# Kernel tuning notes

Hardware: AMD Instinct MI355X
Metric: run time of the kernel (lower is better)

## Reference

```python
import jax, jax.numpy as jnp
import numpy as np

NUM_QUBITS = 24
NUM_QUBITS_GATE = 2
NUM_STEPS = 8
GATE_DIM = 2 ** NUM_QUBITS_GATE  # 4


def setup_inputs() -> dict:
    key = jax.random.key(0)
    k1, k2 = jax.random.split(key)
    # state: stacked (real, imag) parts, shape (2,) + (2,)*NUM_QUBITS
    state = jax.random.normal(k1, (2,) + (2,) * NUM_QUBITS, dtype=jnp.float32)
    state = state / jnp.sqrt(jnp.sum(state * state))  # normalize amplitudes
    # gates: per-step complex 4x4 matrices as stacked (real, imag)
    gates = jax.random.normal(k2, (NUM_STEPS, 2, GATE_DIM, GATE_DIM), dtype=jnp.float32)
    # targets: two distinct qubit indices per step (deterministic, in-range)
    targets = np.array([[s % NUM_QUBITS, (s + 7) % NUM_QUBITS] for s in range(NUM_STEPS)], dtype=np.int64)
    return {"state": state, "gates": gates, "targets": jnp.asarray(targets)}


def _apply_circuit(state, gates, targets_np, n, g):
    G = 2 ** g
    dims = list(range(n))
    for step in range(targets_np.shape[0]):
        target = [int(q) for q in targets_np[step]]
        target_axes = [n - 1 - q for q in target]
        target_axes = list(reversed(target_axes))
        permutation = [i for i in dims if i not in target_axes] + target_axes
        permutation = [0] + [i + 1 for i in permutation]  # keep complex axis first
        inv_permutation = [0] * (n + 1)
        for i, d in enumerate(permutation):
            inv_permutation[d] = i
        # bring target qubit axes to the end, flatten the rest
        st = jnp.transpose(state, permutation).reshape(2, -1, G)  # (2, B, G)
        gr, gi = gates[step, 0], gates[step, 1]  # (G, G) real/imag
        sr, si = st[0], st[1]                    # (B, G)
        # complex matmul: out = gate @ s  (s laid out as (B, G) -> s @ gate.T)
        out_r = sr @ gr.T - si @ gi.T
        out_i = sr @ gi.T + si @ gr.T
        out = jnp.stack([out_r, out_i])          # (2, B, G)
        state = jnp.transpose(out.reshape((2,) + (2,) * n), inv_permutation)
    return state


def reference(state, gates, targets):
    targets_np = np.asarray(targets)  # concrete indices drive the (static) permutations
    return _apply_circuit(state, gates, targets_np, NUM_QUBITS, NUM_QUBITS_GATE)
```

## Files before the change

kernel.cpp:

```cpp
#include <hip/hip_runtime.h>

#define NSTATE (1 << 24)

__device__ __forceinline__ int padi2(int a) { return a + ((a >> 4) << 1); }

__device__ __forceinline__ void cgemv4(float2& x0, float2& x1, float2& x2, float2& x3,
                                       const float* __restrict__ gr,
                                       const float* __restrict__ gi) {
    float2 xs[4] = {x0, x1, x2, x3};
    float2 y[4];
#pragma unroll
    for (int o = 0; o < 4; ++o) {
        float yr = 0.f, yi = 0.f;
#pragma unroll
        for (int h = 0; h < 4; ++h) {
            float a = gr[o * 4 + h], b = gi[o * 4 + h];
            yr = fmaf(a, xs[h].x, yr);
            yr = fmaf(-b, xs[h].y, yr);
            yi = fmaf(a, xs[h].y, yi);
            yi = fmaf(b, xs[h].x, yi);
        }
        y[o] = make_float2(yr, yi);
    }
    x0 = y[0]; x1 = y[1]; x2 = y[2]; x3 = y[3];
}

__device__ __forceinline__ void fused_pair(float2 x[16], const float* __restrict__ gA,
                                           const float* __restrict__ gB) {
#pragma unroll
    for (int m3 = 0; m3 < 2; ++m3)
#pragma unroll
        for (int m1 = 0; m1 < 2; ++m1) {
            const int b = (m1 << 1) | (m3 << 3);
            cgemv4(x[b], x[b | 1], x[b | 4], x[b | 5], gA, gA + 16);
        }
#pragma unroll
    for (int m2 = 0; m2 < 2; ++m2)
#pragma unroll
        for (int m0 = 0; m0 < 2; ++m0) {
            const int b = m0 | (m2 << 2);
            cgemv4(x[b], x[b | 2], x[b | 8], x[b | 10], gB, gB + 16);
        }
}

__global__ void __launch_bounds__(256) qsim_passA(const float* __restrict__ in,
                                                  float* __restrict__ out,
                                                  const float* __restrict__ gates) {
    __shared__ alignas(16) float2 amp[4096 + 512];
    const int tid  = threadIdx.x;
    const int base = blockIdx.x << 12;
#pragma unroll
    for (int k = 0; k < 4; ++k) {
        int t = (tid + (k << 8)) << 2;
        float4 r = *(const float4*)(in + base + t);
        float4 m = *(const float4*)(in + NSTATE + base + t);
        float4* d = (float4*)&amp[padi2(t)];
        d[0] = make_float4(r.x, m.x, r.y, m.y);
        d[1] = make_float4(r.z, m.z, r.w, m.w);
    }
    __syncthreads();
    {
        const int a0 = ((tid & 31) << 2) | ((tid >> 5) << 9);
        float2 x[16];
#pragma unroll
        for (int r = 0; r < 4; ++r) {
            int a = a0 + ((r & 1) << 7) + ((r >> 1) << 8);
            const float4* s = (const float4*)&amp[padi2(a)];
            float4 v0 = s[0], v1 = s[1];
            x[4 * r + 0] = make_float2(v0.x, v0.y);
            x[4 * r + 1] = make_float2(v0.z, v0.w);
            x[4 * r + 2] = make_float2(v1.x, v1.y);
            x[4 * r + 3] = make_float2(v1.z, v1.w);
        }
        fused_pair(x, gates + 0 * 32, gates + 1 * 32);
#pragma unroll
        for (int r = 0; r < 4; ++r) {
            int a = a0 + ((r & 1) << 7) + ((r >> 1) << 8);
            float4* d = (float4*)&amp[padi2(a)];
            d[0] = make_float4(x[4 * r + 0].x, x[4 * r + 0].y, x[4 * r + 1].x, x[4 * r + 1].y);
            d[1] = make_float4(x[4 * r + 2].x, x[4 * r + 2].y, x[4 * r + 3].x, x[4 * r + 3].y);
        }
    }
    __syncthreads();
    {
        const int a0 = (tid & 3) | (((tid >> 2) & 31) << 4) | ((tid >> 7) << 11);
        float2 x[16];
#pragma unroll
        for (int m = 0; m < 16; ++m) {
            int a = a0 | ((m & 1) << 2) | (((m >> 1) & 1) << 3)
                       | (((m >> 2) & 1) << 9) | ((m >> 3) << 10);
            x[m] = amp[padi2(a)];
        }
        fused_pair(x, gates + 2 * 32, gates + 3 * 32);
#pragma unroll
        for (int m = 0; m < 16; ++m) {
            int a = a0 | ((m & 1) << 2) | (((m >> 1) & 1) << 3)
                       | (((m >> 2) & 1) << 9) | ((m >> 3) << 10);
            amp[padi2(a)] = x[m];
        }
    }
    __syncthreads();
#pragma unroll
    for (int k = 0; k < 4; ++k) {
        int t = (tid + (k << 8)) << 2;
        const float4* s = (const float4*)&amp[padi2(t)];
        float4 v0 = s[0], v1 = s[1];
        *(float4*)(out + base + t)          = make_float4(v0.x, v0.z, v1.x, v1.z);
        *(float4*)(out + NSTATE + base + t) = make_float4(v0.y, v0.w, v1.y, v1.w);
    }
}

__global__ void __launch_bounds__(256) qsim_passB(const float* __restrict__ in,
                                                  float* __restrict__ out,
                                                  const float* __restrict__ gates) {
    __shared__ alignas(16) float2 amp[4096 + 512];
    const int tid = threadIdx.x;
    const int bid = blockIdx.x;
    const int base = ((bid & 7) << 8) | ((bid >> 3) << 15);
#pragma unroll
    for (int k = 0; k < 4; ++k) {
        int c = (k << 2) + (tid >> 6);
        int j = (tid & 63) << 2;
        int t = (c << 8) + j;
        int ga = base + (c << 11) + j;
        float4 r = *(const float4*)(in + ga);
        float4 m = *(const float4*)(in + NSTATE + ga);
        float4* d = (float4*)&amp[padi2(t)];
        d[0] = make_float4(r.x, m.x, r.y, m.y);
        d[1] = make_float4(r.z, m.z, r.w, m.w);
    }
    __syncthreads();
    {
        const int a0 = (tid & 15) | (((tid >> 4) & 3) << 6) | ((tid >> 6) << 10);
        float2 x[16];
#pragma unroll
        for (int m = 0; m < 16; ++m) {
            int a = a0 | ((m & 1) << 4) | (((m >> 1) & 1) << 5)
                       | (((m >> 2) & 1) << 8) | ((m >> 3) << 9);
            x[m] = amp[padi2(a)];
        }
        fused_pair(x, gates + 4 * 32, gates + 5 * 32);
#pragma unroll
        for (int m = 0; m < 16; ++m) {
            int a = a0 | ((m & 1) << 4) | (((m >> 1) & 1) << 5)
                       | (((m >> 2) & 1) << 8) | ((m >> 3) << 9);
            amp[padi2(a)] = x[m];
        }
    }
    __syncthreads();
    {
        const int a0 = (tid & 63) | ((tid >> 6) << 8);
        float2 x[16];
#pragma unroll
        for (int m = 0; m < 16; ++m) {
            int a = a0 | ((m & 1) << 6) | (((m >> 1) & 1) << 7)
                       | (((m >> 2) & 1) << 10) | ((m >> 3) << 11);
            x[m] = amp[padi2(a)];
        }
        fused_pair(x, gates + 6 * 32, gates + 7 * 32);
#pragma unroll
        for (int m = 0; m < 16; ++m) {
            int a = a0 | ((m & 1) << 6) | (((m >> 1) & 1) << 7)
                       | (((m >> 2) & 1) << 10) | ((m >> 3) << 11);
            amp[padi2(a)] = x[m];
        }
    }
    __syncthreads();
#pragma unroll
    for (int k = 0; k < 4; ++k) {
        int c = (k << 2) + (tid >> 6);
        int j = (tid & 63) << 2;
        int t = (c << 8) + j;
        int ga = base + (c << 11) + j;
        const float4* s = (const float4*)&amp[padi2(t)];
        float4 v0 = s[0], v1 = s[1];
        *(float4*)(out + ga)          = make_float4(v0.x, v0.z, v1.x, v1.z);
        *(float4*)(out + NSTATE + ga) = make_float4(v0.y, v0.w, v1.y, v1.w);
    }
}

extern "C" void kernel_launch(void* const* d_in, const int* in_sizes, int n_in,
                              void* d_out, int out_size, void* d_ws, size_t ws_size,
                              hipStream_t stream) {
    const float* state = (const float*)d_in[0];
    const float* gates = (const float*)d_in[1];
    float* out = (float*)d_out;
    hipLaunchKernelGGL(qsim_passA, dim3(4096), dim3(256), 0, stream, state, out, gates);
    hipLaunchKernelGGL(qsim_passB, dim3(4096), dim3(256), 0, stream, out, out, gates);
}
```

Baseline: 278.4 us.

## Replace LDS padding with XOR swizzle and halve pass-A tile size

Replaces the padded shared-memory indexing with an XOR swizzle on bits 1-3, keyed by bits 4-6, so the LDS arrays shrink to exactly the tile size and bank conflicts are still avoided without extra storage. Pass A now processes 2048-amplitude tiles with 128 threads, since its gates only touch qubits inside the low 11 bits, and it launches twice as many blocks. The smaller LDS footprint may allow more resident blocks per CU. The risk is that the swizzle pattern conflicts on some of the access strides, and smaller blocks add scheduling overhead.

```diff
diff --git a/kernel.cpp b/kernel.cpp
--- a/kernel.cpp
+++ b/kernel.cpp
@@ -2,7 +2,9 @@
 
 #define NSTATE (1 << 24)
 
-__device__ __forceinline__ int padi2(int a) { return a + ((a >> 4) << 1); }
+__device__ __forceinline__ int swz(int a) {
+    return a ^ (((a >> 4) & 7) << 1);
+}
 
 __device__ __forceinline__ void cgemv4(float2& x0, float2& x1, float2& x2, float2& x3,
                                        const float* __restrict__ gr,
@@ -43,20 +45,19 @@
         }
 }
 
-__global__ void __launch_bounds__(256) qsim_passA(const float* __restrict__ in,
+__global__ void __launch_bounds__(128) qsim_passA(const float* __restrict__ in,
                                                   float* __restrict__ out,
                                                   const float* __restrict__ gates) {
-    __shared__ alignas(16) float2 amp[4096 + 512];
+    __shared__ alignas(16) float2 amp[2048];
     const int tid  = threadIdx.x;
-    const int base = blockIdx.x << 12;
+    const int base = blockIdx.x << 11;
 #pragma unroll
     for (int k = 0; k < 4; ++k) {
-        int t = (tid + (k << 8)) << 2;
+        int t = (tid + (k << 7)) << 2;
         float4 r = *(const float4*)(in + base + t);
         float4 m = *(const float4*)(in + NSTATE + base + t);
-        float4* d = (float4*)&amp[padi2(t)];
-        d[0] = make_float4(r.x, m.x, r.y, m.y);
-        d[1] = make_float4(r.z, m.z, r.w, m.w);
+        *(float4*)&amp[swz(t)]     = make_float4(r.x, m.x, r.y, m.y);
+        *(float4*)&amp[swz(t + 2)] = make_float4(r.z, m.z, r.w, m.w);
     }
     __syncthreads();
     {
@@ -65,8 +66,8 @@
 #pragma unroll
         for (int r = 0; r < 4; ++r) {
             int a = a0 + ((r & 1) << 7) + ((r >> 1) << 8);
-            const float4* s = (const float4*)&amp[padi2(a)];
-            float4 v0 = s[0], v1 = s[1];
+            float4 v0 = *(const float4*)&amp[swz(a)];
+            float4 v1 = *(const float4*)&amp[swz(a + 2)];
             x[4 * r + 0] = make_float2(v0.x, v0.y);
             x[4 * r + 1] = make_float2(v0.z, v0.w);
             x[4 * r + 2] = make_float2(v1.x, v1.y);
@@ -76,35 +77,36 @@
 #pragma unroll
         for (int r = 0; r < 4; ++r) {
             int a = a0 + ((r & 1) << 7) + ((r >> 1) << 8);
-            float4* d = (float4*)&amp[padi2(a)];
-            d[0] = make_float4(x[4 * r + 0].x, x[4 * r + 0].y, x[4 * r + 1].x, x[4 * r + 1].y);
-            d[1] = make_float4(x[4 * r + 2].x, x[4 * r + 2].y, x[4 * r + 3].x, x[4 * r + 3].y);
+            *(float4*)&amp[swz(a)] =
+                make_float4(x[4 * r + 0].x, x[4 * r + 0].y, x[4 * r + 1].x, x[4 * r + 1].y);
+            *(float4*)&amp[swz(a + 2)] =
+                make_float4(x[4 * r + 2].x, x[4 * r + 2].y, x[4 * r + 3].x, x[4 * r + 3].y);
         }
     }
     __syncthreads();
     {
-        const int a0 = (tid & 3) | (((tid >> 2) & 31) << 4) | ((tid >> 7) << 11);
+        const int a0 = (tid & 3) | ((tid >> 2) << 4);
         float2 x[16];
 #pragma unroll
         for (int m = 0; m < 16; ++m) {
             int a = a0 | ((m & 1) << 2) | (((m >> 1) & 1) << 3)
                        | (((m >> 2) & 1) << 9) | ((m >> 3) << 10);
-            x[m] = amp[padi2(a)];
+            x[m] = amp[swz(a)];
         }
         fused_pair(x, gates + 2 * 32, gates + 3 * 32);
 #pragma unroll
         for (int m = 0; m < 16; ++m) {
             int a = a0 | ((m & 1) << 2) | (((m >> 1) & 1) << 3)
                        | (((m >> 2) & 1) << 9) | ((m >> 3) << 10);
-            amp[padi2(a)] = x[m];
+            amp[swz(a)] = x[m];
         }
     }
     __syncthreads();
 #pragma unroll
     for (int k = 0; k < 4; ++k) {
-        int t = (tid + (k << 8)) << 2;
-        const float4* s = (const float4*)&amp[padi2(t)];
-        float4 v0 = s[0], v1 = s[1];
+        int t = (tid + (k << 7)) << 2;
+        float4 v0 = *(const float4*)&amp[swz(t)];
+        float4 v1 = *(const float4*)&amp[swz(t + 2)];
         *(float4*)(out + base + t)          = make_float4(v0.x, v0.z, v1.x, v1.z);
         *(float4*)(out + NSTATE + base + t) = make_float4(v0.y, v0.w, v1.y, v1.w);
     }
@@ -113,7 +115,7 @@
 __global__ void __launch_bounds__(256) qsim_passB(const float* __restrict__ in,
                                                   float* __restrict__ out,
                                                   const float* __restrict__ gates) {
-    __shared__ alignas(16) float2 amp[4096 + 512];
+    __shared__ alignas(16) float2 amp[4096];
     const int tid = threadIdx.x;
     const int bid = blockIdx.x;
     const int base = ((bid & 7) << 8) | ((bid >> 3) << 15);
@@ -125,9 +127,8 @@
         int ga = base + (c << 11) + j;
         float4 r = *(const float4*)(in + ga);
         float4 m = *(const float4*)(in + NSTATE + ga);
-        float4* d = (float4*)&amp[padi2(t)];
-        d[0] = make_float4(r.x, m.x, r.y, m.y);
-        d[1] = make_float4(r.z, m.z, r.w, m.w);
+        *(float4*)&amp[swz(t)]     = make_float4(r.x, m.x, r.y, m.y);
+        *(float4*)&amp[swz(t + 2)] = make_float4(r.z, m.z, r.w, m.w);
     }
     __syncthreads();
     {
@@ -137,14 +138,14 @@
         for (int m = 0; m < 16; ++m) {
             int a = a0 | ((m & 1) << 4) | (((m >> 1) & 1) << 5)
                        | (((m >> 2) & 1) << 8) | ((m >> 3) << 9);
-            x[m] = amp[padi2(a)];
+            x[m] = amp[swz(a)];
         }
         fused_pair(x, gates + 4 * 32, gates + 5 * 32);
 #pragma unroll
         for (int m = 0; m < 16; ++m) {
             int a = a0 | ((m & 1) << 4) | (((m >> 1) & 1) << 5)
                        | (((m >> 2) & 1) << 8) | ((m >> 3) << 9);
-            amp[padi2(a)] = x[m];
+            amp[swz(a)] = x[m];
         }
     }
     __syncthreads();
@@ -155,14 +156,14 @@
         for (int m = 0; m < 16; ++m) {
             int a = a0 | ((m & 1) << 6) | (((m >> 1) & 1) << 7)
                        | (((m >> 2) & 1) << 10) | ((m >> 3) << 11);
-            x[m] = amp[padi2(a)];
+            x[m] = amp[swz(a)];
         }
         fused_pair(x, gates + 6 * 32, gates + 7 * 32);
 #pragma unroll
         for (int m = 0; m < 16; ++m) {
             int a = a0 | ((m & 1) << 6) | (((m >> 1) & 1) << 7)
                        | (((m >> 2) & 1) << 10) | ((m >> 3) << 11);
-            amp[padi2(a)] = x[m];
+            amp[swz(a)] = x[m];
         }
     }
     __syncthreads();
@@ -172,8 +173,8 @@
         int j = (tid & 63) << 2;
         int t = (c << 8) + j;
         int ga = base + (c << 11) + j;
-        const float4* s = (const float4*)&amp[padi2(t)];
-        float4 v0 = s[0], v1 = s[1];
+        float4 v0 = *(const float4*)&amp[swz(t)];
+        float4 v1 = *(const float4*)&amp[swz(t + 2)];
         *(float4*)(out + ga)          = make_float4(v0.x, v0.z, v1.x, v1.z);
         *(float4*)(out + NSTATE + ga) = make_float4(v0.y, v0.w, v1.y, v1.w);
     }
@@ -185,6 +186,6 @@
     const float* state = (const float*)d_in[0];
     const float* gates = (const float*)d_in[1];
     float* out = (float*)d_out;
-    hipLaunchKernelGGL(qsim_passA, dim3(4096), dim3(256), 0, stream, state, out, gates);
+    hipLaunchKernelGGL(qsim_passA, dim3(8192), dim3(128), 0, stream, state, out, gates);
     hipLaunchKernelGGL(qsim_passB, dim3(4096), dim3(256), 0, stream, out, out, gates);
 }
```

After: 280.1 us. Within noise of the previous version (+0.6%).
